# Optimization experiments

Measured on AMD Instinct MI355X. Metric: run time of the kernel, lower is better.

## Reference

```python
import jax, jax.numpy as jnp
import numpy as np

H = 16
N_JOBS = 1000000
N_MACH = 500000
NEG = -1e8

PARAM_SHAPES = [("jW1",(H,H)),("jb1",(H,)),("jW2",(H,H)),("jb2",(H,)),
                ("mW1",(H,H)),("mb1",(H,)),("mW2",(H,H)),("mb2",(H,)),
                ("aj_Wq",(H,H)),("aj_bq",(H,)),("aj_Wr",(H,H)),("aj_V",(H,)),
                ("am_Wq",(H,H)),("am_bq",(H,)),("am_Wr",(H,H)),("am_V",(H,)),
                ("ja_Wq",(H,H)),("ja_bq",(H,)),("ja_Wr",(H,H)),("ja_V",(H,)),
                ("ma_Wq",(H,H)),("ma_bq",(H,)),("ma_Wr",(H,H)),("ma_V",(H,)),
                ("g1W",(H,3*H)),("g1b",(H,)),("g2W",(H,3*H)),("g2b",(H,)),
                ("last_j",(H,))]

def setup_inputs() -> dict:
    key = jax.random.key(0)
    inp = {}
    inp["jobs"] = jax.random.normal(jax.random.fold_in(key, 0), (N_JOBS, H), dtype=jnp.float32)
    inp["machines"] = jax.random.normal(jax.random.fold_in(key, 1), (N_MACH, H), dtype=jnp.float32)
    inp["alloc_jobs_mask"] = jax.random.randint(jax.random.fold_in(key, 2), (N_JOBS,), 0, 2) > 0
    for i, (name, shape) in enumerate(PARAM_SHAPES):
        inp[name] = jax.random.normal(jax.random.fold_in(key, 10 + i), shape, dtype=jnp.float32) * 0.05
    return inp

def _emb(x, W1, b1, W2, b2):
    # custom_embedding: two tanh MLP layers (torch Linear: x @ W.T + b)
    h = jnp.tanh(x @ W1.T + b1)
    return jnp.tanh(h @ W2.T + b2)

def _att_logits(q, ref, Wq, bq, Wr, V):
    # Bahdanau additive attention: tanh(W_q q + W_r ref) @ V -> [S]
    return jnp.tanh((q @ Wq.T + bq) + ref @ Wr.T) @ V

def _query_att(q, ref, Wq, bq, Wr, V):
    # Attention with use_softmax=True followed by weighted sum over ref
    w = jax.nn.softmax(_att_logits(q, ref, Wq, bq, Wr, V))
    return w @ ref  # [H]

def reference(jobs, machines, alloc_jobs_mask,
              jW1, jb1, jW2, jb2, mW1, mb1, mW2, mb2,
              aj_Wq, aj_bq, aj_Wr, aj_V, am_Wq, am_bq, am_Wr, am_V,
              ja_Wq, ja_bq, ja_Wr, ja_V, ma_Wq, ma_bq, ma_Wr, ma_V,
              g1W, g1b, g2W, g2b, last_j):
    E_j = _emb(jobs, jW1, jb1, jW2, jb2)        # [Sj, H]
    E_m = _emb(machines, mW1, mb1, mW2, mb2)    # [Sm, H]

    # glimpse 1 conditioned on last_j
    g_j1 = _query_att(last_j, E_j, aj_Wq, aj_bq, aj_Wr, aj_V)
    g_m1 = _query_att(last_j, E_m, am_Wq, am_bq, am_Wr, am_V)
    g1 = jnp.tanh(jnp.concatenate([last_j, g_j1, g_m1]) @ g1W.T + g1b)

    # job pointer logits + invalid-action masking
    j_logits = _att_logits(g1, E_j, ja_Wq, ja_bq, ja_Wr, ja_V)
    j_logits = jnp.where(alloc_jobs_mask, j_logits, NEG)
    sel_j = jnp.argmax(j_logits)
    e_js = E_j[sel_j]

    # glimpse 2 conditioned on selected job embedding
    g_j2 = _query_att(e_js, E_j, aj_Wq, aj_bq, aj_Wr, aj_V)
    g_m2 = _query_att(e_js, E_m, am_Wq, am_bq, am_Wr, am_V)
    g2 = jnp.tanh(jnp.concatenate([e_js, g_j2, g_m2]) @ g2W.T + g2b)

    m_logits = _att_logits(g2, E_m, ma_Wq, ma_bq, ma_Wr, ma_V)
    sel_m = jnp.argmax(m_logits)

    logpas = jax.nn.log_softmax(j_logits)[sel_j] + jax.nn.log_softmax(m_logits)[sel_m]
    return sel_j, sel_m, logpas
```

## Files before the change

### kernel.cpp

```cpp
#include <hip/hip_runtime.h>
#include <cstddef>
#include <cstdint>


constexpr int NJ = 1000000;
constexpr int NM = 500000;
constexpr float NEGV = -1e8f;

constexpr int BLK = 256;
constexpr int ROWS_PER_BLK = 1024;
constexpr int GB_J = (NJ + ROWS_PER_BLK - 1) / ROWS_PER_BLK;
constexpr int GB_M = (NM + ROWS_PER_BLK - 1) / ROWS_PER_BLK;
constexpr int GB_TOT = GB_J + GB_M;
constexpr int EBLK = ROWS_PER_BLK * 16;

constexpr int S_QKJA = 0;
constexpr int S_QK2J = 16;
constexpr int S_QK2M = 32;
constexpr int S_EJS  = 48;
constexpr int S_QKMA = 64;
constexpr int S_LOGPJ = 80;
constexpr int S_SELJ  = 81;
constexpr int P1J = 128;
constexpr int P1M = P1J + GB_J * 17;
constexpr int P2V = P1M + GB_M * 17;
constexpr int P2I = P2V + GB_J;
constexpr int P2L = P2I + GB_J;
constexpr size_t E_OFF = 65536;
static_assert(P2L + GB_J <= (int)E_OFF, "partials overflow into E cache");
static_assert(NJ % 4 == 0 && NM % 4 == 0, "4-row packing needs n % 4 == 0");

typedef float v2f __attribute__((ext_vector_type(2)));

struct Params {
    const float *jobs, *machines;
    const int *mask;
    const float *jW1, *jb1, *jW2, *jb2;
    const float *mW1, *mb1, *mW2, *mb2;
    const float *aj_Wq, *aj_bq, *aj_Wr, *aj_V;
    const float *am_Wq, *am_bq, *am_Wr, *am_V;
    const float *ja_Wq, *ja_bq, *ja_Wr, *ja_V;
    const float *ma_Wq, *ma_bq, *ma_Wr, *ma_V;
    const float *g1W, *g1b, *g2W, *g2b, *last_j;
    float *S;
    float *Ej, *Em;
    float *out;
};


__device__ __forceinline__ float fast_tanh(float x) {
    float e = __builtin_amdgcn_exp2f(x * 2.8853900817779268f);
    float r = __builtin_amdgcn_rcpf(e + 1.0f);
    return fmaf(-2.0f, r, 1.0f);
}

__device__ __forceinline__ v2f vbc(float a) { v2f r; r.x = a; r.y = a; return r; }

__device__ __forceinline__ v2f vfma(float w, v2f b, v2f c) {
    return __builtin_elementwise_fma(vbc(w), b, c);
}
__device__ __forceinline__ v2f vfma2(v2f a, v2f b, v2f c) {
    return __builtin_elementwise_fma(a, b, c);
}
__device__ __forceinline__ v2f vtanh(v2f a) {
    v2f r; r.x = fast_tanh(a.x); r.y = fast_tanh(a.y); return r;
}

__device__ __forceinline__ void load16(const float* __restrict__ X, size_t r, float (&x)[16]) {
    const float4* p4 = reinterpret_cast<const float4*>(X) + r * 4;
    float4 a = p4[0], b = p4[1], c = p4[2], d = p4[3];
    x[0]=a.x; x[1]=a.y; x[2]=a.z; x[3]=a.w;
    x[4]=b.x; x[5]=b.y; x[6]=b.z; x[7]=b.w;
    x[8]=c.x; x[9]=c.y; x[10]=c.z; x[11]=c.w;
    x[12]=d.x; x[13]=d.y; x[14]=d.z; x[15]=d.w;
}

__device__ __forceinline__ void load16_v2(const float* __restrict__ X, size_t rA, size_t rB,
                                          v2f (&x)[16]) {
    float a[16], b[16];
    load16(X, rA, a);
    load16(X, rB, b);
#pragma unroll
    for (int k = 0; k < 16; ++k) { x[k].x = a[k]; x[k].y = b[k]; }
}

__device__ __forceinline__ void ecache_store4(float* __restrict__ Eb, int t,
                                              const v2f (&e0)[16], const v2f (&e1)[16]) {
    float4* p4 = reinterpret_cast<float4*>(Eb);
#pragma unroll
    for (int kp = 0; kp < 8; ++kp) {
        p4[kp * 512 + t]       = make_float4(e0[2*kp].x, e0[2*kp].y, e0[2*kp+1].x, e0[2*kp+1].y);
        p4[kp * 512 + 256 + t] = make_float4(e1[2*kp].x, e1[2*kp].y, e1[2*kp+1].x, e1[2*kp+1].y);
    }
}
__device__ __forceinline__ void ecache_load4(const float* __restrict__ Eb, int t,
                                             v2f (&e0)[16], v2f (&e1)[16]) {
    const float4* p4 = reinterpret_cast<const float4*>(Eb);
#pragma unroll
    for (int kp = 0; kp < 8; ++kp) {
        float4 q0 = p4[kp * 512 + t];
        float4 q1 = p4[kp * 512 + 256 + t];
        e0[2*kp].x = q0.x;   e0[2*kp].y = q0.y;
        e0[2*kp+1].x = q0.z; e0[2*kp+1].y = q0.w;
        e1[2*kp].x = q1.x;   e1[2*kp].y = q1.y;
        e1[2*kp+1].x = q1.z; e1[2*kp+1].y = q1.w;
    }
}

__device__ __forceinline__ void emb16_v2(const v2f (&x)[16],
                                         const float* __restrict__ W1, const float* __restrict__ b1,
                                         const float* __restrict__ W2, const float* __restrict__ b2,
                                         v2f (&e)[16]) {
    v2f h[16];
#pragma unroll
    for (int i = 0; i < 16; ++i) {
        v2f a = vbc(b1[i]);
#pragma unroll
        for (int k = 0; k < 16; ++k) a = vfma(W1[i * 16 + k], x[k], a);
        h[i] = vtanh(a);
    }
#pragma unroll
    for (int i = 0; i < 16; ++i) {
        v2f a = vbc(b2[i]);
#pragma unroll
        for (int k = 0; k < 16; ++k) a = vfma(W2[i * 16 + k], h[k], a);
        e[i] = vtanh(a);
    }
}

__device__ __forceinline__ v2f att_logit_v2(const v2f (&e)[16], const float (&qk)[16],
                                            const float* __restrict__ Wr,
                                            const float* __restrict__ V) {
    v2f acc = vbc(0.0f);
#pragma unroll
    for (int i = 0; i < 16; ++i) {
        v2f r = vbc(qk[i]);
#pragma unroll
        for (int k = 0; k < 16; ++k) r = vfma(Wr[i * 16 + k], e[k], r);
        acc = vfma2(vbc(V[i]), vtanh(r), acc);
    }
    return acc;
}

__device__ __forceinline__ float wave_reduce_sum(float v) {
#pragma unroll
    for (int off = 32; off > 0; off >>= 1) v += __shfl_xor(v, off, 64);
    return v;
}

__device__ __forceinline__ void wave_reduce_argmax(float &v, int &idx) {
#pragma unroll
    for (int off = 32; off > 0; off >>= 1) {
        float ov = __shfl_xor(v, off, 64);
        int oi = __shfl_xor(idx, off, 64);
        if (ov > v || (ov == v && oi < idx)) { v = ov; idx = oi; }
    }
}

__device__ __forceinline__ float block_sum(float v) {
    __shared__ float sm[4];
    v = wave_reduce_sum(v);
    __syncthreads();
    if ((threadIdx.x & 63) == 0) sm[threadIdx.x >> 6] = v;
    __syncthreads();
    return sm[0] + sm[1] + sm[2] + sm[3];
}

__device__ __forceinline__ void block_argmax(float &v, int &i) {
    __shared__ float sv[4];
    __shared__ int si[4];
    wave_reduce_argmax(v, i);
    __syncthreads();
    if ((threadIdx.x & 63) == 0) { sv[threadIdx.x >> 6] = v; si[threadIdx.x >> 6] = i; }
    __syncthreads();
    float bv = sv[0]; int bi = si[0];
#pragma unroll
    for (int k = 1; k < 4; ++k)
        if (sv[k] > bv || (sv[k] == bv && si[k] < bi)) { bv = sv[k]; bi = si[k]; }
    v = bv; i = bi;
}

__device__ __forceinline__ void block_sum17(float l, const float (&s)[16], float* dst) {
    const int lane = threadIdx.x & 63;
    float c[8];
#pragma unroll
    for (int j = 0; j < 8; ++j) {
        const bool hi = lane & 1;
        float t = __shfl_xor(hi ? s[j] : s[j + 8], 1, 64);
        c[j] = (hi ? s[j + 8] : s[j]) + t;
    }
    float d[4];
#pragma unroll
    for (int j = 0; j < 4; ++j) {
        const bool hi = lane & 2;
        float t = __shfl_xor(hi ? c[j] : c[j + 4], 2, 64);
        d[j] = (hi ? c[j + 4] : c[j]) + t;
    }
    float e2[2];
#pragma unroll
    for (int j = 0; j < 2; ++j) {
        const bool hi = lane & 4;
        float t = __shfl_xor(hi ? d[j] : d[j + 2], 4, 64);
        e2[j] = (hi ? d[j + 2] : d[j]) + t;
    }
    float f;
    {
        const bool hi = lane & 8;
        float t = __shfl_xor(hi ? e2[0] : e2[1], 8, 64);
        f = (hi ? e2[1] : e2[0]) + t;
    }
    f += __shfl_xor(f, 16, 64);
    f += __shfl_xor(f, 32, 64);
#pragma unroll
    for (int off = 32; off > 0; off >>= 1) l += __shfl_xor(l, off, 64);

    const int idx = ((lane & 1) << 3) | ((lane & 2) << 1) | ((lane & 4) >> 1) | ((lane & 8) >> 3);
    __shared__ float red[4][17];
    const int w = threadIdx.x >> 6;
    __syncthreads();
    if (lane < 16) red[w][1 + idx] = f;
    if (lane == 0) red[w][0] = l;
    __syncthreads();
    if (threadIdx.x < 17)
        dst[threadIdx.x] = red[0][threadIdx.x] + red[1][threadIdx.x] + red[2][threadIdx.x] + red[3][threadIdx.x];
}

__device__ __forceinline__ void wsum4(const v2f (&e0)[16], const v2f (&e1)[16],
                                      v2f w01, v2f w23, float (&s)[16]) {
#pragma unroll
    for (int i = 0; i < 16; ++i) {
        v2f t = vfma2(w23, e1[i], w01 * e0[i]);
        s[i] = t.x + t.y;
    }
}

template <bool CACHE>
__global__ __launch_bounds__(BLK) void k_emb_g1(Params p) {
    const bool isJob = blockIdx.x < GB_J;
    const float* X  = isJob ? p.jobs : p.machines;
    const float* W1 = isJob ? p.jW1 : p.mW1;
    const float* b1 = isJob ? p.jb1 : p.mb1;
    const float* W2 = isJob ? p.jW2 : p.mW2;
    const float* b2 = isJob ? p.jb2 : p.mb2;
    const float* Wr = isJob ? p.aj_Wr : p.am_Wr;
    const float* V  = isJob ? p.aj_V  : p.am_V;
    float* E = isJob ? p.Ej : p.Em;
    const int n  = isJob ? NJ : NM;
    const int b0 = isJob ? (int)blockIdx.x : (int)blockIdx.x - GB_J;

    const int r0 = b0 * ROWS_PER_BLK + 4 * (int)threadIdx.x;
    const bool v = r0 < n;
    const size_t a0 = v ? (size_t)r0 : 0;
    const size_t d  = v ? 1 : 0;

    v2f x0[16], x1[16];
    load16_v2(X, a0, a0 + d, x0);
    load16_v2(X, a0 + 2 * d, a0 + 3 * d, x1);

    __shared__ float qks[16];
    if (threadIdx.x < 16) {
        const float* Wq = isJob ? p.aj_Wq : p.am_Wq;
        const float* bq = isJob ? p.aj_bq : p.am_bq;
        const int i = threadIdx.x;
        float a = bq[i];
#pragma unroll
        for (int k = 0; k < 16; ++k) a = fmaf(Wq[i * 16 + k], p.last_j[k], a);
        qks[i] = a;
    }
    __syncthreads();
    float qk[16];
#pragma unroll
    for (int i = 0; i < 16; ++i) qk[i] = qks[i];

    v2f e0[16], e1[16];
    emb16_v2(x0, W1, b1, W2, b2, e0);
    emb16_v2(x1, W1, b1, W2, b2, e1);
    if (CACHE) ecache_store4(E + (size_t)b0 * EBLK, (int)threadIdx.x, e0, e1);
    v2f lg0 = att_logit_v2(e0, qk, Wr, V);
    v2f lg1 = att_logit_v2(e1, qk, Wr, V);
    v2f w01, w23;
    w01.x = v ? __expf(lg0.x) : 0.0f;
    w01.y = v ? __expf(lg0.y) : 0.0f;
    w23.x = v ? __expf(lg1.x) : 0.0f;
    w23.y = v ? __expf(lg1.y) : 0.0f;
    float l = (w01.x + w01.y) + (w23.x + w23.y);
    float s[16];
    wsum4(e0, e1, w01, w23, s);

    block_sum17(l, s, p.S + (isJob ? P1J : P1M) + (size_t)b0 * 17);
}

__global__ __launch_bounds__(BLK) void k_combine_g(Params p, int phase) {
    const float* PJ = p.S + P1J;
    const float* PM = p.S + P1M;
    float lJ = 0.0f, lM = 0.0f, sJ[16], sM[16];
#pragma unroll
    for (int c = 0; c < 16; ++c) { sJ[c] = 0.0f; sM[c] = 0.0f; }
    for (int i = threadIdx.x; i < GB_J; i += BLK) {
        lJ += PJ[i * 17];
#pragma unroll
        for (int c = 0; c < 16; ++c) sJ[c] += PJ[i * 17 + 1 + c];
    }
    for (int i = threadIdx.x; i < GB_M; i += BLK) {
        lM += PM[i * 17];
#pragma unroll
        for (int c = 0; c < 16; ++c) sM[c] += PM[i * 17 + 1 + c];
    }
    __shared__ float totJ[17], totM[17];
    block_sum17(lJ, sJ, totJ);
    block_sum17(lM, sM, totM);
    __syncthreads();

    __shared__ float cb[48], gbuf[16];
    if (threadIdx.x < 16) {
        int i = threadIdx.x;
        cb[i]      = phase ? p.S[S_EJS + i] : p.last_j[i];
        cb[16 + i] = totJ[1 + i] / totJ[0];
        cb[32 + i] = totM[1 + i] / totM[0];
    }
    __syncthreads();
    const float* gW  = phase ? p.g2W : p.g1W;
    const float* gbv = phase ? p.g2b : p.g1b;
    if (threadIdx.x < 16) {
        int i = threadIdx.x;
        float a = gbv[i];
#pragma unroll
        for (int k = 0; k < 48; ++k) a = fmaf(gW[i * 48 + k], cb[k], a);
        gbuf[i] = fast_tanh(a);
    }
    __syncthreads();
    const float* Wq = phase ? p.ma_Wq : p.ja_Wq;
    const float* bq = phase ? p.ma_bq : p.ja_bq;
    const int off = phase ? S_QKMA : S_QKJA;
    if (threadIdx.x < 16) {
        int i = threadIdx.x;
        float a = bq[i];
#pragma unroll
        for (int k = 0; k < 16; ++k) a = fmaf(Wq[i * 16 + k], gbuf[k], a);
        p.S[off + i] = a;
    }
}

template <bool CACHE>
__global__ __launch_bounds__(BLK) void k_jlogits(Params p) {
    const int r0 = blockIdx.x * ROWS_PER_BLK + 4 * (int)threadIdx.x;
    const bool v = r0 < NJ;
    const size_t a0 = v ? (size_t)r0 : 0;
    const size_t d  = v ? 1 : 0;

    int4 mq = make_int4(0, 0, 0, 0);
    if (v) mq = *reinterpret_cast<const int4*>(p.mask + r0);

    v2f e0[16], e1[16];
    if (CACHE) {
        ecache_load4(p.Ej + (size_t)blockIdx.x * EBLK, (int)threadIdx.x, e0, e1);
    } else {
        v2f x0[16], x1[16];
        load16_v2(p.jobs, a0, a0 + d, x0);
        load16_v2(p.jobs, a0 + 2 * d, a0 + 3 * d, x1);
        emb16_v2(x0, p.jW1, p.jb1, p.jW2, p.jb2, e0);
        emb16_v2(x1, p.jW1, p.jb1, p.jW2, p.jb2, e1);
    }
    float qk[16];
#pragma unroll
    for (int i = 0; i < 16; ++i) qk[i] = p.S[S_QKJA + i];

    v2f lg0 = att_logit_v2(e0, qk, p.ja_Wr, p.ja_V);
    v2f lg1 = att_logit_v2(e1, qk, p.ja_Wr, p.ja_V);

    const bool m0 = v && (mq.x != 0);
    const bool m1 = v && (mq.y != 0);
    const bool m2 = v && (mq.z != 0);
    const bool m3 = v && (mq.w != 0);
    float l = (m0 ? __expf(lg0.x) : 0.0f) + (m1 ? __expf(lg0.y) : 0.0f)
            + (m2 ? __expf(lg1.x) : 0.0f) + (m3 ? __expf(lg1.y) : 0.0f);
    float am0 = m0 ? lg0.x : NEGV - 1.0f;
    float am1 = m1 ? lg0.y : NEGV - 1.0f;
    float am2 = m2 ? lg1.x : NEGV - 1.0f;
    float am3 = m3 ? lg1.y : NEGV - 1.0f;
    float best = am0; int bi = r0;
    if (am1 > best) { best = am1; bi = r0 + 1; }
    if (am2 > best) { best = am2; bi = r0 + 2; }
    if (am3 > best) { best = am3; bi = r0 + 3; }

    l = wave_reduce_sum(l);
    wave_reduce_argmax(best, bi);
    __shared__ float rl[4], rv[4];
    __shared__ int ri[4];
    int w = threadIdx.x >> 6, ln = threadIdx.x & 63;
    if (ln == 0) { rl[w] = l; rv[w] = best; ri[w] = bi; }
    __syncthreads();
    if (threadIdx.x == 0) {
        float L = rl[0] + rl[1] + rl[2] + rl[3];
        float vv = rv[0]; int i = ri[0];
#pragma unroll
        for (int k = 1; k < 4; ++k)
            if (rv[k] > vv || (rv[k] == vv && ri[k] < i)) { vv = rv[k]; i = ri[k]; }
        p.S[P2V + blockIdx.x] = vv;
        p.S[P2I + blockIdx.x] = (float)i;
        p.S[P2L + blockIdx.x] = L;
    }
}

__global__ __launch_bounds__(BLK) void k_combine2(Params p) {
    float v = -3.4e38f; int vi = 0x7fffffff; float l = 0.0f;
    for (int i = threadIdx.x; i < GB_J; i += BLK) {
        float pv = p.S[P2V + i];
        int pi = (int)p.S[P2I + i];
        if (pv > v || (pv == v && pi < vi)) { v = pv; vi = pi; }
        l += p.S[P2L + i];
    }
    l = block_sum(l);
    block_argmax(v, vi);
    const int sel = vi;

    __shared__ float xb[16], hb[16], eb[16];
    if (threadIdx.x < 16) xb[threadIdx.x] = p.jobs[(size_t)sel * 16 + threadIdx.x];
    __syncthreads();
    if (threadIdx.x < 16) {
        int i = threadIdx.x;
        float a = p.jb1[i];
#pragma unroll
        for (int k = 0; k < 16; ++k) a = fmaf(p.jW1[i * 16 + k], xb[k], a);
        hb[i] = fast_tanh(a);
    }
    __syncthreads();
    if (threadIdx.x < 16) {
        int i = threadIdx.x;
        float a = p.jb2[i];
#pragma unroll
        for (int k = 0; k < 16; ++k) a = fmaf(p.jW2[i * 16 + k], hb[k], a);
        float e = fast_tanh(a);
        eb[i] = e;
        p.S[S_EJS + i] = e;
    }
    __syncthreads();
    if (threadIdx.x < 16) {
        int i = threadIdx.x;
        float a1 = p.aj_bq[i], a2 = p.am_bq[i];
#pragma unroll
        for (int k = 0; k < 16; ++k) {
            a1 = fmaf(p.aj_Wq[i * 16 + k], eb[k], a1);
            a2 = fmaf(p.am_Wq[i * 16 + k], eb[k], a2);
        }
        p.S[S_QK2J + i] = a1;
        p.S[S_QK2M + i] = a2;
    }
    if (threadIdx.x == 0) {
        p.S[S_LOGPJ] = v - logf(l);
        p.S[S_SELJ] = (float)sel;
    }
}

template <bool CACHE>
__global__ __launch_bounds__(BLK) void k_glimpse2(Params p) {
    const bool isJob = blockIdx.x < GB_J;
    const float* Wr = isJob ? p.aj_Wr : p.am_Wr;
    const float* V  = isJob ? p.aj_V  : p.am_V;
    const float* E  = isJob ? p.Ej : p.Em;
    const float* X  = isJob ? p.jobs : p.machines;
    const float* W1 = isJob ? p.jW1 : p.mW1;
    const float* b1 = isJob ? p.jb1 : p.mb1;
    const float* W2 = isJob ? p.jW2 : p.mW2;
    const float* b2 = isJob ? p.jb2 : p.mb2;
    const int n  = isJob ? NJ : NM;
    const int b0 = isJob ? (int)blockIdx.x : (int)blockIdx.x - GB_J;
    const int qoff = isJob ? S_QK2J : S_QK2M;

    const int r0 = b0 * ROWS_PER_BLK + 4 * (int)threadIdx.x;
    const bool v = r0 < n;
    const size_t a0 = v ? (size_t)r0 : 0;
    const size_t d  = v ? 1 : 0;

    v2f e0[16], e1[16];
    if (CACHE) {
        ecache_load4(E + (size_t)b0 * EBLK, (int)threadIdx.x, e0, e1);
    } else {
        v2f x0[16], x1[16];
        load16_v2(X, a0, a0 + d, x0);
        load16_v2(X, a0 + 2 * d, a0 + 3 * d, x1);
        emb16_v2(x0, W1, b1, W2, b2, e0);
        emb16_v2(x1, W1, b1, W2, b2, e1);
    }
    float qk[16];
#pragma unroll
    for (int i = 0; i < 16; ++i) qk[i] = p.S[qoff + i];

    v2f lg0 = att_logit_v2(e0, qk, Wr, V);
    v2f lg1 = att_logit_v2(e1, qk, Wr, V);
    v2f w01, w23;
    w01.x = v ? __expf(lg0.x) : 0.0f;
    w01.y = v ? __expf(lg0.y) : 0.0f;
    w23.x = v ? __expf(lg1.x) : 0.0f;
    w23.y = v ? __expf(lg1.y) : 0.0f;
    float l = (w01.x + w01.y) + (w23.x + w23.y);
    float s[16];
    wsum4(e0, e1, w01, w23, s);

    block_sum17(l, s, p.S + (isJob ? P1J : P1M) + (size_t)b0 * 17);
}

template <bool CACHE>
__global__ __launch_bounds__(BLK) void k_mlogits(Params p) {
    const int r0 = blockIdx.x * ROWS_PER_BLK + 4 * (int)threadIdx.x;
    const bool v = r0 < NM;
    const size_t a0 = v ? (size_t)r0 : 0;
    const size_t d  = v ? 1 : 0;

    v2f e0[16], e1[16];
    if (CACHE) {
        ecache_load4(p.Em + (size_t)blockIdx.x * EBLK, (int)threadIdx.x, e0, e1);
    } else {
        v2f x0[16], x1[16];
        load16_v2(p.machines, a0, a0 + d, x0);
        load16_v2(p.machines, a0 + 2 * d, a0 + 3 * d, x1);
        emb16_v2(x0, p.mW1, p.mb1, p.mW2, p.mb2, e0);
        emb16_v2(x1, p.mW1, p.mb1, p.mW2, p.mb2, e1);
    }
    float qk[16];
#pragma unroll
    for (int i = 0; i < 16; ++i) qk[i] = p.S[S_QKMA + i];

    v2f lg0 = att_logit_v2(e0, qk, p.ma_Wr, p.ma_V);
    v2f lg1 = att_logit_v2(e1, qk, p.ma_Wr, p.ma_V);
    float l = (v ? __expf(lg0.x) : 0.0f) + (v ? __expf(lg0.y) : 0.0f)
            + (v ? __expf(lg1.x) : 0.0f) + (v ? __expf(lg1.y) : 0.0f);
    float am0 = v ? lg0.x : -3.4e38f;
    float am1 = v ? lg0.y : -3.4e38f;
    float am2 = v ? lg1.x : -3.4e38f;
    float am3 = v ? lg1.y : -3.4e38f;
    float best = am0; int bi = r0;
    if (am1 > best) { best = am1; bi = r0 + 1; }
    if (am2 > best) { best = am2; bi = r0 + 2; }
    if (am3 > best) { best = am3; bi = r0 + 3; }

    l = wave_reduce_sum(l);
    wave_reduce_argmax(best, bi);
    __shared__ float rl[4], rv[4];
    __shared__ int ri[4];
    int w = threadIdx.x >> 6, ln = threadIdx.x & 63;
    if (ln == 0) { rl[w] = l; rv[w] = best; ri[w] = bi; }
    __syncthreads();
    if (threadIdx.x == 0) {
        float L = rl[0] + rl[1] + rl[2] + rl[3];
        float vv = rv[0]; int i = ri[0];
#pragma unroll
        for (int k = 1; k < 4; ++k)
            if (rv[k] > vv || (rv[k] == vv && ri[k] < i)) { vv = rv[k]; i = ri[k]; }
        p.S[P2V + blockIdx.x] = vv;
        p.S[P2I + blockIdx.x] = (float)i;
        p.S[P2L + blockIdx.x] = L;
    }
}

__global__ __launch_bounds__(BLK) void k_combine4(Params p) {
    float v = -3.4e38f; int vi = 0x7fffffff; float l = 0.0f;
    for (int i = threadIdx.x; i < GB_M; i += BLK) {
        float pv = p.S[P2V + i];
        int pi = (int)p.S[P2I + i];
        if (pv > v || (pv == v && pi < vi)) { v = pv; vi = pi; }
        l += p.S[P2L + i];
    }
    l = block_sum(l);
    block_argmax(v, vi);
    if (threadIdx.x == 0) {
        p.out[0] = p.S[S_SELJ];
        p.out[1] = (float)vi;
        p.out[2] = p.S[S_LOGPJ] + (v - logf(l));
    }
}

extern "C" void kernel_launch(void* const* d_in, const int* in_sizes, int n_in,
                              void* d_out, int out_size, void* d_ws, size_t ws_size,
                              hipStream_t stream) {
    Params p;
    p.jobs     = (const float*)d_in[0];
    p.machines = (const float*)d_in[1];
    p.mask     = (const int*)d_in[2];
    p.jW1 = (const float*)d_in[3];  p.jb1 = (const float*)d_in[4];
    p.jW2 = (const float*)d_in[5];  p.jb2 = (const float*)d_in[6];
    p.mW1 = (const float*)d_in[7];  p.mb1 = (const float*)d_in[8];
    p.mW2 = (const float*)d_in[9];  p.mb2 = (const float*)d_in[10];
    p.aj_Wq = (const float*)d_in[11]; p.aj_bq = (const float*)d_in[12];
    p.aj_Wr = (const float*)d_in[13]; p.aj_V  = (const float*)d_in[14];
    p.am_Wq = (const float*)d_in[15]; p.am_bq = (const float*)d_in[16];
    p.am_Wr = (const float*)d_in[17]; p.am_V  = (const float*)d_in[18];
    p.ja_Wq = (const float*)d_in[19]; p.ja_bq = (const float*)d_in[20];
    p.ja_Wr = (const float*)d_in[21]; p.ja_V  = (const float*)d_in[22];
    p.ma_Wq = (const float*)d_in[23]; p.ma_bq = (const float*)d_in[24];
    p.ma_Wr = (const float*)d_in[25]; p.ma_V  = (const float*)d_in[26];
    p.g1W = (const float*)d_in[27]; p.g1b = (const float*)d_in[28];
    p.g2W = (const float*)d_in[29]; p.g2b = (const float*)d_in[30];
    p.last_j = (const float*)d_in[31];
    p.S = (float*)d_ws;
    p.Ej = (float*)d_ws + E_OFF;
    p.Em = p.Ej + (size_t)GB_J * EBLK;
    p.out = (float*)d_out;

    const size_t needed = (E_OFF + (size_t)GB_TOT * EBLK) * sizeof(float);
    const bool cache = ws_size >= needed;

    if (cache) {
        k_emb_g1<true><<<GB_TOT, BLK, 0, stream>>>(p);
        k_combine_g<<<1, BLK, 0, stream>>>(p, 0);
        k_jlogits<true><<<GB_J, BLK, 0, stream>>>(p);
        k_combine2<<<1, BLK, 0, stream>>>(p);
        k_glimpse2<true><<<GB_TOT, BLK, 0, stream>>>(p);
        k_combine_g<<<1, BLK, 0, stream>>>(p, 1);
        k_mlogits<true><<<GB_M, BLK, 0, stream>>>(p);
        k_combine4<<<1, BLK, 0, stream>>>(p);
    } else {
        k_emb_g1<false><<<GB_TOT, BLK, 0, stream>>>(p);
        k_combine_g<<<1, BLK, 0, stream>>>(p, 0);
        k_jlogits<false><<<GB_J, BLK, 0, stream>>>(p);
        k_combine2<<<1, BLK, 0, stream>>>(p);
        k_glimpse2<false><<<GB_TOT, BLK, 0, stream>>>(p);
        k_combine_g<<<1, BLK, 0, stream>>>(p, 1);
        k_mlogits<false><<<GB_M, BLK, 0, stream>>>(p);
        k_combine4<<<1, BLK, 0, stream>>>(p);
    }
}
```

Measured before the change: 283.5 us.

## Precompute pointer-attention Wr·E projections in first pass and cache them

In the first embedding pass, the ja_Wr/ma_Wr projections of every job and machine embedding are computed and written to a second workspace cache. The job-logit and machine-logit kernels then load these projections and only add the query and apply tanh·V, skipping the 16x16 matvec. This trades compute in the logit kernels for an extra 96 MB of writes plus reads and more work in the first kernel. The new path is taken only when the workspace is large enough.

```diff
diff --git a/kernel.cpp b/kernel.cpp
--- a/kernel.cpp
+++ b/kernel.cpp
@@ -44,6 +44,7 @@
     const float *g1W, *g1b, *g2W, *g2b, *last_j;
     float *S;
     float *Ej, *Em;
+    float *Wj, *Wm;
     float *out;
 };
 
@@ -142,6 +143,30 @@
     return acc;
 }
 
+__device__ __forceinline__ v2f att_logit_pre(const v2f (&wr)[16], const float (&qk)[16],
+                                             const float* __restrict__ V) {
+    v2f acc = vbc(0.0f);
+#pragma unroll
+    for (int i = 0; i < 16; ++i)
+        acc = vfma2(vbc(V[i]), vtanh(vbc(qk[i]) + wr[i]), acc);
+    return acc;
+}
+
+__device__ __forceinline__ void wr_mv2(const v2f (&e0)[16], const v2f (&e1)[16],
+                                       const float* __restrict__ Wr,
+                                       v2f (&w0)[16], v2f (&w1)[16]) {
+#pragma unroll
+    for (int i = 0; i < 16; ++i) {
+        v2f a = vbc(0.0f), b = vbc(0.0f);
+#pragma unroll
+        for (int k = 0; k < 16; ++k) {
+            a = vfma(Wr[i * 16 + k], e0[k], a);
+            b = vfma(Wr[i * 16 + k], e1[k], b);
+        }
+        w0[i] = a; w1[i] = b;
+    }
+}
+
 __device__ __forceinline__ float wave_reduce_sum(float v) {
 #pragma unroll
     for (int off = 32; off > 0; off >>= 1) v += __shfl_xor(v, off, 64);
@@ -234,7 +259,7 @@
     }
 }
 
-template <bool CACHE>
+template <int TIER>
 __global__ __launch_bounds__(BLK) void k_emb_g1(Params p) {
     const bool isJob = blockIdx.x < GB_J;
     const float* X  = isJob ? p.jobs : p.machines;
@@ -244,7 +269,6 @@
     const float* b2 = isJob ? p.jb2 : p.mb2;
     const float* Wr = isJob ? p.aj_Wr : p.am_Wr;
     const float* V  = isJob ? p.aj_V  : p.am_V;
-    float* E = isJob ? p.Ej : p.Em;
     const int n  = isJob ? NJ : NM;
     const int b0 = isJob ? (int)blockIdx.x : (int)blockIdx.x - GB_J;
 
@@ -275,7 +299,14 @@
     v2f e0[16], e1[16];
     emb16_v2(x0, W1, b1, W2, b2, e0);
     emb16_v2(x1, W1, b1, W2, b2, e1);
-    if (CACHE) ecache_store4(E + (size_t)b0 * EBLK, (int)threadIdx.x, e0, e1);
+    if (TIER >= 1)
+        ecache_store4((isJob ? p.Ej : p.Em) + (size_t)b0 * EBLK, (int)threadIdx.x, e0, e1);
+    if (TIER == 2) {
+        const float* WrX = isJob ? p.ja_Wr : p.ma_Wr;
+        v2f w0[16], w1[16];
+        wr_mv2(e0, e1, WrX, w0, w1);
+        ecache_store4((isJob ? p.Wj : p.Wm) + (size_t)b0 * EBLK, (int)threadIdx.x, w0, w1);
+    }
     v2f lg0 = att_logit_v2(e0, qk, Wr, V);
     v2f lg1 = att_logit_v2(e1, qk, Wr, V);
     v2f w01, w23;
@@ -341,7 +372,7 @@
     }
 }
 
-template <bool CACHE>
+template <int TIER>
 __global__ __launch_bounds__(BLK) void k_jlogits(Params p) {
     const int r0 = blockIdx.x * ROWS_PER_BLK + 4 * (int)threadIdx.x;
     const bool v = r0 < NJ;
@@ -351,22 +382,30 @@
     int4 mq = make_int4(0, 0, 0, 0);
     if (v) mq = *reinterpret_cast<const int4*>(p.mask + r0);
 
-    v2f e0[16], e1[16];
-    if (CACHE) {
+    float qk[16];
+#pragma unroll
+    for (int i = 0; i < 16; ++i) qk[i] = p.S[S_QKJA + i];
+
+    v2f lg0, lg1;
+    if (TIER == 2) {
+        v2f w0[16], w1[16];
+        ecache_load4(p.Wj + (size_t)blockIdx.x * EBLK, (int)threadIdx.x, w0, w1);
+        lg0 = att_logit_pre(w0, qk, p.ja_V);
+        lg1 = att_logit_pre(w1, qk, p.ja_V);
+    } else if (TIER == 1) {
+        v2f e0[16], e1[16];
         ecache_load4(p.Ej + (size_t)blockIdx.x * EBLK, (int)threadIdx.x, e0, e1);
+        lg0 = att_logit_v2(e0, qk, p.ja_Wr, p.ja_V);
+        lg1 = att_logit_v2(e1, qk, p.ja_Wr, p.ja_V);
     } else {
-        v2f x0[16], x1[16];
+        v2f x0[16], x1[16], e0[16], e1[16];
         load16_v2(p.jobs, a0, a0 + d, x0);
         load16_v2(p.jobs, a0 + 2 * d, a0 + 3 * d, x1);
         emb16_v2(x0, p.jW1, p.jb1, p.jW2, p.jb2, e0);
         emb16_v2(x1, p.jW1, p.jb1, p.jW2, p.jb2, e1);
-    }
-    float qk[16];
-#pragma unroll
-    for (int i = 0; i < 16; ++i) qk[i] = p.S[S_QKJA + i];
-
-    v2f lg0 = att_logit_v2(e0, qk, p.ja_Wr, p.ja_V);
-    v2f lg1 = att_logit_v2(e1, qk, p.ja_Wr, p.ja_V);
+        lg0 = att_logit_v2(e0, qk, p.ja_Wr, p.ja_V);
+        lg1 = att_logit_v2(e1, qk, p.ja_Wr, p.ja_V);
+    }
 
     const bool m0 = v && (mq.x != 0);
     const bool m1 = v && (mq.y != 0);
@@ -500,29 +539,38 @@
     block_sum17(l, s, p.S + (isJob ? P1J : P1M) + (size_t)b0 * 17);
 }
 
-template <bool CACHE>
+template <int TIER>
 __global__ __launch_bounds__(BLK) void k_mlogits(Params p) {
     const int r0 = blockIdx.x * ROWS_PER_BLK + 4 * (int)threadIdx.x;
     const bool v = r0 < NM;
     const size_t a0 = v ? (size_t)r0 : 0;
     const size_t d  = v ? 1 : 0;
 
-    v2f e0[16], e1[16];
-    if (CACHE) {
+    float qk[16];
+#pragma unroll
+    for (int i = 0; i < 16; ++i) qk[i] = p.S[S_QKMA + i];
+
+    v2f lg0, lg1;
+    if (TIER == 2) {
+        v2f w0[16], w1[16];
+        ecache_load4(p.Wm + (size_t)blockIdx.x * EBLK, (int)threadIdx.x, w0, w1);
+        lg0 = att_logit_pre(w0, qk, p.ma_V);
+        lg1 = att_logit_pre(w1, qk, p.ma_V);
+    } else if (TIER == 1) {
+        v2f e0[16], e1[16];
         ecache_load4(p.Em + (size_t)blockIdx.x * EBLK, (int)threadIdx.x, e0, e1);
+        lg0 = att_logit_v2(e0, qk, p.ma_Wr, p.ma_V);
+        lg1 = att_logit_v2(e1, qk, p.ma_Wr, p.ma_V);
     } else {
-        v2f x0[16], x1[16];
+        v2f x0[16], x1[16], e0[16], e1[16];
         load16_v2(p.machines, a0, a0 + d, x0);
         load16_v2(p.machines, a0 + 2 * d, a0 + 3 * d, x1);
         emb16_v2(x0, p.mW1, p.mb1, p.mW2, p.mb2, e0);
         emb16_v2(x1, p.mW1, p.mb1, p.mW2, p.mb2, e1);
-    }
-    float qk[16];
-#pragma unroll
-    for (int i = 0; i < 16; ++i) qk[i] = p.S[S_QKMA + i];
-
-    v2f lg0 = att_logit_v2(e0, qk, p.ma_Wr, p.ma_V);
-    v2f lg1 = att_logit_v2(e1, qk, p.ma_Wr, p.ma_V);
+        lg0 = att_logit_v2(e0, qk, p.ma_Wr, p.ma_V);
+        lg1 = att_logit_v2(e1, qk, p.ma_Wr, p.ma_V);
+    }
+
     float l = (v ? __expf(lg0.x) : 0.0f) + (v ? __expf(lg0.y) : 0.0f)
             + (v ? __expf(lg1.x) : 0.0f) + (v ? __expf(lg1.y) : 0.0f);
     float am0 = v ? lg0.x : -3.4e38f;
@@ -595,28 +643,40 @@
     p.S = (float*)d_ws;
     p.Ej = (float*)d_ws + E_OFF;
     p.Em = p.Ej + (size_t)GB_J * EBLK;
+    p.Wj = p.Ej + (size_t)GB_TOT * EBLK;
+    p.Wm = p.Wj + (size_t)GB_J * EBLK;
     p.out = (float*)d_out;
 
-    const size_t needed = (E_OFF + (size_t)GB_TOT * EBLK) * sizeof(float);
-    const bool cache = ws_size >= needed;
-
-    if (cache) {
-        k_emb_g1<true><<<GB_TOT, BLK, 0, stream>>>(p);
+    const size_t need_e    = (E_OFF + (size_t)GB_TOT * EBLK) * sizeof(float);
+    const size_t need_full = (E_OFF + 2 * (size_t)GB_TOT * EBLK) * sizeof(float);
+    const int tier = (ws_size >= need_full) ? 2 : (ws_size >= need_e ? 1 : 0);
+
+    if (tier == 2) {
+        k_emb_g1<2><<<GB_TOT, BLK, 0, stream>>>(p);
         k_combine_g<<<1, BLK, 0, stream>>>(p, 0);
-        k_jlogits<true><<<GB_J, BLK, 0, stream>>>(p);
+        k_jlogits<2><<<GB_J, BLK, 0, stream>>>(p);
         k_combine2<<<1, BLK, 0, stream>>>(p);
         k_glimpse2<true><<<GB_TOT, BLK, 0, stream>>>(p);
         k_combine_g<<<1, BLK, 0, stream>>>(p, 1);
-        k_mlogits<true><<<GB_M, BLK, 0, stream>>>(p);
+        k_mlogits<2><<<GB_M, BLK, 0, stream>>>(p);
+        k_combine4<<<1, BLK, 0, stream>>>(p);
+    } else if (tier == 1) {
+        k_emb_g1<1><<<GB_TOT, BLK, 0, stream>>>(p);
+        k_combine_g<<<1, BLK, 0, stream>>>(p, 0);
+        k_jlogits<1><<<GB_J, BLK, 0, stream>>>(p);
+        k_combine2<<<1, BLK, 0, stream>>>(p);
+        k_glimpse2<true><<<GB_TOT, BLK, 0, stream>>>(p);
+        k_combine_g<<<1, BLK, 0, stream>>>(p, 1);
+        k_mlogits<1><<<GB_M, BLK, 0, stream>>>(p);
         k_combine4<<<1, BLK, 0, stream>>>(p);
     } else {
-        k_emb_g1<false><<<GB_TOT, BLK, 0, stream>>>(p);
+        k_emb_g1<0><<<GB_TOT, BLK, 0, stream>>>(p);
         k_combine_g<<<1, BLK, 0, stream>>>(p, 0);
-        k_jlogits<false><<<GB_J, BLK, 0, stream>>>(p);
+        k_jlogits<0><<<GB_J, BLK, 0, stream>>>(p);
         k_combine2<<<1, BLK, 0, stream>>>(p);
         k_glimpse2<false><<<GB_TOT, BLK, 0, stream>>>(p);
         k_combine_g<<<1, BLK, 0, stream>>>(p, 1);
-        k_mlogits<false><<<GB_M, BLK, 0, stream>>>(p);
+        k_mlogits<0><<<GB_M, BLK, 0, stream>>>(p);
         k_combine4<<<1, BLK, 0, stream>>>(p);
     }
 }
```

New measurement: 328.5 us. 15.9% more time.
